# Kernel tuning notes

Measured on AMD Instinct MI355X. Metric: run time of the kernel, lower is better.

Reference implementation:

```python
import jax, jax.numpy as jnp
import numpy as np

HEAD_SIZE = 64
N_EMBD = 768

def setup_inputs() -> dict:
    key = jax.random.key(0)
    kx, kq, kk, kv = jax.random.split(key, 4)
    x = jax.random.normal(kx, (4, 4096, N_EMBD), dtype=jnp.float32)
    s = 1.0 / np.sqrt(N_EMBD)
    Wq = jax.random.normal(kq, (N_EMBD, HEAD_SIZE), dtype=jnp.float32) * s
    Wk = jax.random.normal(kk, (N_EMBD, HEAD_SIZE), dtype=jnp.float32) * s
    Wv = jax.random.normal(kv, (N_EMBD, HEAD_SIZE), dtype=jnp.float32) * s
    return {"x": x, "Wq": Wq, "Wk": Wk, "Wv": Wv}

def reference(x, Wq, Wk, Wv):
    b, t, c = x.shape
    h = Wq.shape[1]
    q = jnp.einsum('btc,ch->bth', x, Wq)
    k = jnp.einsum('btc,ch->bth', x, Wk)
    v = jnp.einsum('btc,ch->bth', x, Wv)
    scores = jnp.einsum('bqh,bkh->bqk', q, k) / jnp.sqrt(jnp.float32(h))
    causal = jnp.tril(jnp.ones((t, t), dtype=bool))  # [t,t]
    scores = jnp.where(causal, scores, -jnp.inf)
    attn = jax.nn.softmax(scores, axis=-1)
    return jnp.einsum('bqk,bkh->bqh', attn, v)
```

## Files before the change

### kernel.cpp

```cpp
#include <hip/hip_runtime.h>
#include <math.h>

#define BB 4
#define TT 4096
#define CC 768
#define HH 64
#define NN 192
#define LDP 72
#define GR 32
#define XSTR 776
#define SC2 0.180336880f

typedef __bf16 bf16x8 __attribute__((ext_vector_type(8)));
typedef float floatx4 __attribute__((ext_vector_type(4)));
typedef unsigned short u16x8 __attribute__((ext_vector_type(8)));

__device__ inline unsigned short f2bf(float f) {
    union { __bf16 b; unsigned short u; } v;
    v.b = (__bf16)f;
    return v.u;
}
__device__ inline float bf2f(unsigned short u) {
    union { unsigned int u; float f; } v;
    v.u = (unsigned int)u << 16;
    return v.f;
}

__global__ __launch_bounds__(256) void wprep(const float* __restrict__ Wq,
                                             const float* __restrict__ Wk,
                                             const float* __restrict__ Wv,
                                             unsigned short* __restrict__ wtf) {
    const int idx = blockIdx.x * 256 + threadIdx.x;
    if (idx >= NN * CC) return;
    const int j = idx & 7;
    const int lane = (idx >> 3) & 63;
    const int rest = idx >> 9;
    const int kg = rest % 24;
    const int n_tile = rest / 24;
    const int c = kg * 32 + (lane >> 4) * 8 + j;
    const int n = n_tile * 16 + (lane & 15);
    const float* W = (n < 64) ? Wq : (n < 128) ? Wk : Wv;
    wtf[idx] = f2bf(W[c * HH + (n & 63)]);
}

__global__ __launch_bounds__(256) void qkv_gemm(const float* __restrict__ x,
                                                const unsigned short* __restrict__ wtf,
                                                unsigned short* __restrict__ qb,
                                                unsigned short* __restrict__ kb,
                                                unsigned short* __restrict__ vbt) {
    __shared__ unsigned short As[GR * XSTR];

    const int tid = threadIdx.x;
    const int w = tid >> 6, lane = tid & 63;
    const int l15 = lane & 15, quad = lane >> 4;
    const int m0 = blockIdx.x * GR;
    const int n0 = w * 48;
    const int nt0 = w * 3;

    const float* xbase = x + (size_t)m0 * CC;
#pragma unroll
    for (int e = 0; e < 12; ++e) {
        const int c = tid + 256 * e;
        const int r = c / 96, off = (c - r * 96) * 8;
        const float4 v0 = *(const float4*)(xbase + (size_t)c * 8);
        const float4 v1 = *(const float4*)(xbase + (size_t)c * 8 + 4);
        u16x8 pk;
        pk[0] = f2bf(v0.x); pk[1] = f2bf(v0.y); pk[2] = f2bf(v0.z); pk[3] = f2bf(v0.w);
        pk[4] = f2bf(v1.x); pk[5] = f2bf(v1.y); pk[6] = f2bf(v1.z); pk[7] = f2bf(v1.w);
        *(u16x8*)(As + r * XSTR + off) = pk;
    }
    __syncthreads();

    floatx4 acc[2][3] = {};
#pragma unroll 4
    for (int step = 0; step < 12; ++step) {
        bf16x8 a0[2], a1[2];
#pragma unroll
        for (int rg = 0; rg < 2; ++rg) {
            const unsigned short* ap = As + (16 * rg + l15) * XSTR + step * 64 + quad * 8;
            a0[rg] = *(const bf16x8*)(ap);
            a1[rg] = *(const bf16x8*)(ap + 32);
        }
#pragma unroll
        for (int j = 0; j < 3; ++j) {
            const unsigned short* bp =
                wtf + ((size_t)((nt0 + j) * 24 + 2 * step) * 64 + lane) * 8;
            const bf16x8 b0 = *(const bf16x8*)(bp);
            const bf16x8 b1 = *(const bf16x8*)(bp + 512);
#pragma unroll
            for (int rg = 0; rg < 2; ++rg) {
                acc[rg][j] = __builtin_amdgcn_mfma_f32_16x16x32_bf16(a0[rg], b0, acc[rg][j], 0, 0, 0);
                acc[rg][j] = __builtin_amdgcn_mfma_f32_16x16x32_bf16(a1[rg], b1, acc[rg][j], 0, 0, 0);
            }
        }
    }

    const int b = m0 >> 12;
#pragma unroll
    for (int j = 0; j < 3; ++j) {
        const int n = n0 + j * 16 + l15;
        const int mid = n >> 6;
        const int h = n & 63;
#pragma unroll
        for (int rg = 0; rg < 2; ++rg) {
            const int tloc = (m0 & (TT - 1)) + 16 * rg + quad * 4;
            if (mid == 2) {
                ushort4 pk;
                pk.x = f2bf(acc[rg][j][0]); pk.y = f2bf(acc[rg][j][1]);
                pk.z = f2bf(acc[rg][j][2]); pk.w = f2bf(acc[rg][j][3]);
                *(ushort4*)(vbt + ((size_t)b * HH + h) * TT + tloc) = pk;
            } else {
                unsigned short* dst = (mid == 0) ? qb : kb;
#pragma unroll
                for (int r = 0; r < 4; ++r)
                    dst[(size_t)(m0 + 16 * rg + quad * 4 + r) * HH + h] = f2bf(acc[rg][j][r]);
            }
        }
    }
}

template<int CH>
__global__ __launch_bounds__(256) void attn_part(const unsigned short* __restrict__ qb,
                                                 const unsigned short* __restrict__ kb,
                                                 const unsigned short* __restrict__ vbt,
                                                 unsigned short* __restrict__ Opart,
                                                 float* __restrict__ lsum,
                                                 float* __restrict__ out) {
    __shared__ unsigned short Ks[64 * LDP];
    __shared__ unsigned short VTs[64 * LDP];
    __shared__ unsigned short Ps[4][16 * LDP];

    constexpr int NG = 64 / CH;
    constexpr int TOTB = CH * (NG * (NG + 1)) / 2;

    const int b = blockIdx.x & 3;
    int rem = TOTB - 1 - (blockIdx.x >> 2);
    int g = 0;
    while (rem >= CH * (g + 1)) { rem -= CH * (g + 1); ++g; }
    const int qt = g * CH + rem / (g + 1);
    const int ch = rem - (rem / (g + 1)) * (g + 1);

    const int q0  = qt * 64;
    const int tid = threadIdx.x;
    const int w = tid >> 6, lane = tid & 63;
    const int l15 = lane & 15, quad = lane >> 4;

    const unsigned short* Qb  = qb  + (size_t)b * TT * HH;
    const unsigned short* Kb  = kb  + (size_t)b * TT * HH;
    const unsigned short* VTb = vbt + (size_t)b * HH * TT;

    const int qrow = q0 + 16 * w + l15;
    const bf16x8 qf0 = *(const bf16x8*)(Qb + (size_t)qrow * HH + quad * 8);
    const bf16x8 qf1 = *(const bf16x8*)(Qb + (size_t)qrow * HH + 32 + quad * 8);

    floatx4 O[4] = {};
    floatx4 lacc = {0.f, 0.f, 0.f, 0.f};

    const int kt0 = ch * CH;
    const int kt1 = min(kt0 + CH, qt + 1);
    for (int kt = kt0; kt < kt1; ++kt) {
        __syncthreads();
        const unsigned short* Kt = Kb + (size_t)(kt * 64) * HH;
        const unsigned short* Vt = VTb + kt * 64;
#pragma unroll
        for (int e = 0; e < 2; ++e) {
            const int chunk = tid + 256 * e;
            const int r = chunk >> 3, c0 = (chunk & 7) * 8;
            *(u16x8*)(Ks + r * LDP + c0)  = *(const u16x8*)(Kt + r * HH + c0);
            *(u16x8*)(VTs + r * LDP + c0) = *(const u16x8*)(Vt + (size_t)r * TT + c0);
        }
        __syncthreads();

        floatx4 s[4];
#pragma unroll
        for (int ki = 0; ki < 4; ++ki) {
            const bf16x8 kf0 = *(const bf16x8*)(Ks + (16 * ki + l15) * LDP + quad * 8);
            const bf16x8 kf1 = *(const bf16x8*)(Ks + (16 * ki + l15) * LDP + 32 + quad * 8);
            floatx4 c = {};
            c = __builtin_amdgcn_mfma_f32_16x16x32_bf16(qf0, kf0, c, 0, 0, 0);
            c = __builtin_amdgcn_mfma_f32_16x16x32_bf16(qf1, kf1, c, 0, 0, 0);
            s[ki] = c * SC2;
        }

        if (kt == qt) {
#pragma unroll
            for (int ki = 0; ki < 4; ++ki)
#pragma unroll
                for (int r = 0; r < 4; ++r) {
                    const int kloc = 16 * ki + l15;
                    const int qloc = 16 * w + quad * 4 + r;
                    if (kloc > qloc) s[ki][r] = -INFINITY;
                }
        }

#pragma unroll
        for (int ki = 0; ki < 4; ++ki)
#pragma unroll
            for (int r = 0; r < 4; ++r) {
                const float p = exp2f(s[ki][r]);
                s[ki][r] = p;
                lacc[r] += p;
            }

        unsigned short* Pw = Ps[w];
#pragma unroll
        for (int ki = 0; ki < 4; ++ki)
#pragma unroll
            for (int r = 0; r < 4; ++r)
                Pw[(quad * 4 + r) * LDP + 16 * ki + l15] = f2bf(s[ki][r]);

        const bf16x8 pf0 = *(const bf16x8*)(Pw + l15 * LDP + quad * 8);
        const bf16x8 pf1 = *(const bf16x8*)(Pw + l15 * LDP + 32 + quad * 8);
#pragma unroll
        for (int di = 0; di < 4; ++di) {
            const bf16x8 vf0 = *(const bf16x8*)(VTs + (16 * di + l15) * LDP + quad * 8);
            const bf16x8 vf1 = *(const bf16x8*)(VTs + (16 * di + l15) * LDP + 32 + quad * 8);
            O[di] = __builtin_amdgcn_mfma_f32_16x16x32_bf16(pf0, vf0, O[di], 0, 0, 0);
            O[di] = __builtin_amdgcn_mfma_f32_16x16x32_bf16(pf1, vf1, O[di], 0, 0, 0);
        }
    }

    float l_r[4];
#pragma unroll
    for (int r = 0; r < 4; ++r) {
        float v = lacc[r];
#pragma unroll
        for (int msk = 8; msk >= 1; msk >>= 1) v += __shfl_xor(v, msk, 64);
        l_r[r] = v;
    }

    if (qt < CH) {
        float* outp = out + ((size_t)b * TT + q0 + 16 * w) * HH;
#pragma unroll
        for (int di = 0; di < 4; ++di)
#pragma unroll
            for (int r = 0; r < 4; ++r)
                outp[(quad * 4 + r) * HH + 16 * di + l15] = O[di][r] / l_r[r];
        return;
    }

    const int pbase = ((b * 64 + qt) * NG + ch) * 64;
    unsigned short* Op = Opart + (size_t)pbase * HH + 16 * w * HH;
#pragma unroll
    for (int di = 0; di < 4; ++di)
#pragma unroll
        for (int r = 0; r < 4; ++r)
            Op[(quad * 4 + r) * HH + 16 * di + l15] = f2bf(O[di][r]);
    if (l15 == 0) {
#pragma unroll
        for (int r = 0; r < 4; ++r)
            lsum[pbase + 16 * w + quad * 4 + r] = l_r[r];
    }
}

template<int CH>
__global__ __launch_bounds__(256) void attn_merge(const unsigned short* __restrict__ Opart,
                                                  const float* __restrict__ lsum,
                                                  float* __restrict__ out) {
    constexpr int NG = 64 / CH;
    const int g = blockIdx.x * 256 + threadIdx.x;
    const int row = g >> 3, oct = g & 7;
    const int b = row >> 12, t = row & (TT - 1);
    const int qt = t >> 6, rloc = t & 63;
    if (qt < CH) return;
    const int nchunk = qt / CH + 1;
    const int pbase = ((b * 64 + qt) * NG) * 64 + rloc;
    const int d0 = oct * 8;

    float L = 0.f;
    float a[8] = {};
    for (int c = 0; c < nchunk; ++c) {
        const int idx = pbase + c * 64;
        L += lsum[idx];
        const u16x8 pv = *(const u16x8*)(Opart + (size_t)idx * HH + d0);
#pragma unroll
        for (int k = 0; k < 8; ++k) a[k] += bf2f(pv[k]);
    }
    const float inv = 1.f / L;
    float4 o0, o1;
    o0.x = a[0] * inv; o0.y = a[1] * inv; o0.z = a[2] * inv; o0.w = a[3] * inv;
    o1.x = a[4] * inv; o1.y = a[5] * inv; o1.z = a[6] * inv; o1.w = a[7] * inv;
    float* dst = out + (size_t)row * HH + d0;
    *(float4*)(dst) = o0;
    *(float4*)(dst + 4) = o1;
}

__global__ __launch_bounds__(256) void attn_full(const unsigned short* __restrict__ qb,
                                                 const unsigned short* __restrict__ kb,
                                                 const unsigned short* __restrict__ vbt,
                                                 float* __restrict__ out) {
    __shared__ unsigned short Ks[64 * LDP];
    __shared__ unsigned short VTs[64 * LDP];
    __shared__ unsigned short Ps[4][16 * LDP];

    const int b   = blockIdx.x >> 6;
    const int qt  = blockIdx.x & 63;
    const int q0  = qt * 64;
    const int tid = threadIdx.x;
    const int w = tid >> 6, lane = tid & 63;
    const int l15 = lane & 15, quad = lane >> 4;

    const unsigned short* Qb  = qb  + (size_t)b * TT * HH;
    const unsigned short* Kb  = kb  + (size_t)b * TT * HH;
    const unsigned short* VTb = vbt + (size_t)b * HH * TT;

    const int qrow = q0 + 16 * w + l15;
    const bf16x8 qf0 = *(const bf16x8*)(Qb + (size_t)qrow * HH + quad * 8);
    const bf16x8 qf1 = *(const bf16x8*)(Qb + (size_t)qrow * HH + 32 + quad * 8);

    floatx4 O[4] = {};
    floatx4 lacc = {0.f, 0.f, 0.f, 0.f};

    for (int kt = 0; kt <= qt; ++kt) {
        __syncthreads();
        const unsigned short* Kt = Kb + (size_t)(kt * 64) * HH;
        const unsigned short* Vt = VTb + kt * 64;
#pragma unroll
        for (int e = 0; e < 2; ++e) {
            const int chunk = tid + 256 * e;
            const int r = chunk >> 3, c0 = (chunk & 7) * 8;
            *(u16x8*)(Ks + r * LDP + c0)  = *(const u16x8*)(Kt + r * HH + c0);
            *(u16x8*)(VTs + r * LDP + c0) = *(const u16x8*)(Vt + (size_t)r * TT + c0);
        }
        __syncthreads();

        floatx4 s[4];
#pragma unroll
        for (int ki = 0; ki < 4; ++ki) {
            const bf16x8 kf0 = *(const bf16x8*)(Ks + (16 * ki + l15) * LDP + quad * 8);
            const bf16x8 kf1 = *(const bf16x8*)(Ks + (16 * ki + l15) * LDP + 32 + quad * 8);
            floatx4 c = {};
            c = __builtin_amdgcn_mfma_f32_16x16x32_bf16(qf0, kf0, c, 0, 0, 0);
            c = __builtin_amdgcn_mfma_f32_16x16x32_bf16(qf1, kf1, c, 0, 0, 0);
            s[ki] = c * SC2;
        }
        if (kt == qt) {
#pragma unroll
            for (int ki = 0; ki < 4; ++ki)
#pragma unroll
                for (int r = 0; r < 4; ++r)
                    if (16 * ki + l15 > 16 * w + quad * 4 + r) s[ki][r] = -INFINITY;
        }
#pragma unroll
        for (int ki = 0; ki < 4; ++ki)
#pragma unroll
            for (int r = 0; r < 4; ++r) {
                const float p = exp2f(s[ki][r]);
                s[ki][r] = p; lacc[r] += p;
            }

        unsigned short* Pw = Ps[w];
#pragma unroll
        for (int ki = 0; ki < 4; ++ki)
#pragma unroll
            for (int r = 0; r < 4; ++r)
                Pw[(quad * 4 + r) * LDP + 16 * ki + l15] = f2bf(s[ki][r]);

        const bf16x8 pf0 = *(const bf16x8*)(Pw + l15 * LDP + quad * 8);
        const bf16x8 pf1 = *(const bf16x8*)(Pw + l15 * LDP + 32 + quad * 8);
#pragma unroll
        for (int di = 0; di < 4; ++di) {
            const bf16x8 vf0 = *(const bf16x8*)(VTs + (16 * di + l15) * LDP + quad * 8);
            const bf16x8 vf1 = *(const bf16x8*)(VTs + (16 * di + l15) * LDP + 32 + quad * 8);
            O[di] = __builtin_amdgcn_mfma_f32_16x16x32_bf16(pf0, vf0, O[di], 0, 0, 0);
            O[di] = __builtin_amdgcn_mfma_f32_16x16x32_bf16(pf1, vf1, O[di], 0, 0, 0);
        }
    }
    float l_r[4];
#pragma unroll
    for (int r = 0; r < 4; ++r) {
        float v = lacc[r];
#pragma unroll
        for (int msk = 8; msk >= 1; msk >>= 1) v += __shfl_xor(v, msk, 64);
        l_r[r] = v;
    }
    float* outp = out + ((size_t)b * TT + q0 + 16 * w) * HH;
#pragma unroll
    for (int di = 0; di < 4; ++di)
#pragma unroll
        for (int r = 0; r < 4; ++r)
            outp[(quad * 4 + r) * HH + 16 * di + l15] = O[di][r] / l_r[r];
}

extern "C" void kernel_launch(void* const* d_in, const int* in_sizes, int n_in,
                              void* d_out, int out_size, void* d_ws, size_t ws_size,
                              hipStream_t stream) {
    const float* x  = (const float*)d_in[0];
    const float* Wq = (const float*)d_in[1];
    const float* Wk = (const float*)d_in[2];
    const float* Wv = (const float*)d_in[3];
    float* out = (float*)d_out;

    const size_t nQKV = (size_t)BB * TT * HH;
    unsigned short* qb  = (unsigned short*)d_ws;
    unsigned short* kb  = qb + nQKV;
    unsigned short* vbt = kb + nQKV;
    unsigned short* wtf = vbt + nQKV;
    unsigned short* Opart = wtf + (size_t)NN * CC;

    const size_t prows8  = (size_t)BB * 64 * 8 * 64;
    const size_t prows16 = (size_t)BB * 64 * 4 * 64;
    float* lsum8  = (float*)(Opart + prows8 * HH);
    float* lsum16 = (float*)(Opart + prows16 * HH);
    const size_t need8  = (size_t)((char*)(lsum8  + prows8)  - (char*)d_ws);
    const size_t need16 = (size_t)((char*)(lsum16 + prows16) - (char*)d_ws);

    wprep<<<(NN * CC + 255) / 256, 256, 0, stream>>>(Wq, Wk, Wv, wtf);
    qkv_gemm<<<(BB * TT) / GR, 256, 0, stream>>>(x, wtf, qb, kb, vbt);
    if (ws_size >= need8) {
        attn_part<8><<<BB * 288, 256, 0, stream>>>(qb, kb, vbt, Opart, lsum8, out);
        attn_merge<8><<<(BB * TT * 8) / 256, 256, 0, stream>>>(Opart, lsum8, out);
    } else if (ws_size >= need16) {
        attn_part<16><<<BB * 160, 256, 0, stream>>>(qb, kb, vbt, Opart, lsum16, out);
        attn_merge<16><<<(BB * TT * 8) / 256, 256, 0, stream>>>(Opart, lsum16, out);
    } else {
        attn_full<<<BB * (TT / 64), 256, 0, stream>>>(qb, kb, vbt, out);
    }
}
```

Measured before the change: 130.6 us.

## Load K and V MFMA fragments directly from global memory, dropping LDS staging

Removes the shared-memory staging of K and V tiles and both block-wide barriers per key tile in the attention kernels. Each wave now reads its MFMA operand fragments straight from global memory (through L1/L2). This cuts the LDS round trip and the synchronization, and lowers LDS use, which may allow more resident blocks. In exchange, all four waves load the same K/V data redundantly from global memory, and the V reads stride by TT, so cache pressure and load latency go up with no explicit prefetching.

```diff
diff --git a/kernel.cpp b/kernel.cpp
--- a/kernel.cpp
+++ b/kernel.cpp
@@ -126,8 +126,6 @@
                                                  unsigned short* __restrict__ Opart,
                                                  float* __restrict__ lsum,
                                                  float* __restrict__ out) {
-    __shared__ unsigned short Ks[64 * LDP];
-    __shared__ unsigned short VTs[64 * LDP];
     __shared__ unsigned short Ps[4][16 * LDP];
 
     constexpr int NG = 64 / CH;
@@ -159,23 +157,15 @@
     const int kt0 = ch * CH;
     const int kt1 = min(kt0 + CH, qt + 1);
     for (int kt = kt0; kt < kt1; ++kt) {
-        __syncthreads();
         const unsigned short* Kt = Kb + (size_t)(kt * 64) * HH;
         const unsigned short* Vt = VTb + kt * 64;
-#pragma unroll
-        for (int e = 0; e < 2; ++e) {
-            const int chunk = tid + 256 * e;
-            const int r = chunk >> 3, c0 = (chunk & 7) * 8;
-            *(u16x8*)(Ks + r * LDP + c0)  = *(const u16x8*)(Kt + r * HH + c0);
-            *(u16x8*)(VTs + r * LDP + c0) = *(const u16x8*)(Vt + (size_t)r * TT + c0);
-        }
-        __syncthreads();
 
         floatx4 s[4];
 #pragma unroll
         for (int ki = 0; ki < 4; ++ki) {
-            const bf16x8 kf0 = *(const bf16x8*)(Ks + (16 * ki + l15) * LDP + quad * 8);
-            const bf16x8 kf1 = *(const bf16x8*)(Ks + (16 * ki + l15) * LDP + 32 + quad * 8);
+            const unsigned short* kp = Kt + (size_t)(16 * ki + l15) * HH + quad * 8;
+            const bf16x8 kf0 = *(const bf16x8*)(kp);
+            const bf16x8 kf1 = *(const bf16x8*)(kp + 32);
             floatx4 c = {};
             c = __builtin_amdgcn_mfma_f32_16x16x32_bf16(qf0, kf0, c, 0, 0, 0);
             c = __builtin_amdgcn_mfma_f32_16x16x32_bf16(qf1, kf1, c, 0, 0, 0);
@@ -213,8 +203,9 @@
         const bf16x8 pf1 = *(const bf16x8*)(Pw + l15 * LDP + 32 + quad * 8);
 #pragma unroll
         for (int di = 0; di < 4; ++di) {
-            const bf16x8 vf0 = *(const bf16x8*)(VTs + (16 * di + l15) * LDP + quad * 8);
-            const bf16x8 vf1 = *(const bf16x8*)(VTs + (16 * di + l15) * LDP + 32 + quad * 8);
+            const unsigned short* vp = Vt + (size_t)(16 * di + l15) * TT + quad * 8;
+            const bf16x8 vf0 = *(const bf16x8*)(vp);
+            const bf16x8 vf1 = *(const bf16x8*)(vp + 32);
             O[di] = __builtin_amdgcn_mfma_f32_16x16x32_bf16(pf0, vf0, O[di], 0, 0, 0);
             O[di] = __builtin_amdgcn_mfma_f32_16x16x32_bf16(pf1, vf1, O[di], 0, 0, 0);
         }
@@ -289,8 +280,6 @@
                                                  const unsigned short* __restrict__ kb,
                                                  const unsigned short* __restrict__ vbt,
                                                  float* __restrict__ out) {
-    __shared__ unsigned short Ks[64 * LDP];
-    __shared__ unsigned short VTs[64 * LDP];
     __shared__ unsigned short Ps[4][16 * LDP];
 
     const int b   = blockIdx.x >> 6;
@@ -312,23 +301,15 @@
     floatx4 lacc = {0.f, 0.f, 0.f, 0.f};
 
     for (int kt = 0; kt <= qt; ++kt) {
-        __syncthreads();
         const unsigned short* Kt = Kb + (size_t)(kt * 64) * HH;
         const unsigned short* Vt = VTb + kt * 64;
-#pragma unroll
-        for (int e = 0; e < 2; ++e) {
-            const int chunk = tid + 256 * e;
-            const int r = chunk >> 3, c0 = (chunk & 7) * 8;
-            *(u16x8*)(Ks + r * LDP + c0)  = *(const u16x8*)(Kt + r * HH + c0);
-            *(u16x8*)(VTs + r * LDP + c0) = *(const u16x8*)(Vt + (size_t)r * TT + c0);
-        }
-        __syncthreads();
 
         floatx4 s[4];
 #pragma unroll
         for (int ki = 0; ki < 4; ++ki) {
-            const bf16x8 kf0 = *(const bf16x8*)(Ks + (16 * ki + l15) * LDP + quad * 8);
-            const bf16x8 kf1 = *(const bf16x8*)(Ks + (16 * ki + l15) * LDP + 32 + quad * 8);
+            const unsigned short* kp = Kt + (size_t)(16 * ki + l15) * HH + quad * 8;
+            const bf16x8 kf0 = *(const bf16x8*)(kp);
+            const bf16x8 kf1 = *(const bf16x8*)(kp + 32);
             floatx4 c = {};
             c = __builtin_amdgcn_mfma_f32_16x16x32_bf16(qf0, kf0, c, 0, 0, 0);
             c = __builtin_amdgcn_mfma_f32_16x16x32_bf16(qf1, kf1, c, 0, 0, 0);
@@ -360,8 +341,9 @@
         const bf16x8 pf1 = *(const bf16x8*)(Pw + l15 * LDP + 32 + quad * 8);
 #pragma unroll
         for (int di = 0; di < 4; ++di) {
-            const bf16x8 vf0 = *(const bf16x8*)(VTs + (16 * di + l15) * LDP + quad * 8);
-            const bf16x8 vf1 = *(const bf16x8*)(VTs + (16 * di + l15) * LDP + 32 + quad * 8);
+            const unsigned short* vp = Vt + (size_t)(16 * di + l15) * TT + quad * 8;
+            const bf16x8 vf0 = *(const bf16x8*)(vp);
+            const bf16x8 vf1 = *(const bf16x8*)(vp + 32);
             O[di] = __builtin_amdgcn_mfma_f32_16x16x32_bf16(pf0, vf0, O[di], 0, 0, 0);
             O[di] = __builtin_amdgcn_mfma_f32_16x16x32_bf16(pf1, vf1, O[di], 0, 0, 0);
         }
```

Result: slower. 175.6 us (+34.5%).

## Rework attention partial kernel to 32x32 MFMA with register-resident K/V and split-K waves

Applied to the files above, without the earlier changes.

Replaces the 16x16x32 MFMA attention tile with 32x32x16 MFMAs computing S^T = K·Q^T. K and V fragments now load straight from global memory into registers, with the next K tile prefetched, so the shared-memory staging and the two barriers per tile are gone. P is repacked in registers using packed bf16 converts and a cross-half lane shuffle instead of a shared-memory round trip. The 4 waves are split 2x2 over query and key halves, and their partial O and row sums are reduced through shared memory at the end. This removes LDS traffic and synchronisation, at the cost of redundant global reads of K/V per wave and more register pressure.

```diff
diff --git a/kernel.cpp b/kernel.cpp
--- a/kernel.cpp
+++ b/kernel.cpp
@@ -13,6 +13,7 @@
 
 typedef __bf16 bf16x8 __attribute__((ext_vector_type(8)));
 typedef float floatx4 __attribute__((ext_vector_type(4)));
+typedef float floatx16 __attribute__((ext_vector_type(16)));
 typedef unsigned short u16x8 __attribute__((ext_vector_type(8)));
 
 __device__ inline unsigned short f2bf(float f) {
@@ -24,6 +25,11 @@
     union { unsigned int u; float f; } v;
     v.u = (unsigned int)u << 16;
     return v.f;
+}
+__device__ inline unsigned cvtpk(float lo, float hi) {
+    unsigned d;
+    asm("v_cvt_pk_bf16_f32 %0, %1, %2" : "=v"(d) : "v"(lo), "v"(hi));
+    return d;
 }
 
 __global__ __launch_bounds__(256) void wprep(const float* __restrict__ Wq,
@@ -126,9 +132,8 @@
                                                  unsigned short* __restrict__ Opart,
                                                  float* __restrict__ lsum,
                                                  float* __restrict__ out) {
-    __shared__ unsigned short Ks[64 * LDP];
-    __shared__ unsigned short VTs[64 * LDP];
-    __shared__ unsigned short Ps[4][16 * LDP];
+    __shared__ float Osh[2][2][16][64];
+    __shared__ float Lsh[2][64];
 
     constexpr int NG = 64 / CH;
     constexpr int TOTB = CH * (NG * (NG + 1)) / 2;
@@ -143,114 +148,140 @@
     const int q0  = qt * 64;
     const int tid = threadIdx.x;
     const int w = tid >> 6, lane = tid & 63;
-    const int l15 = lane & 15, quad = lane >> 4;
+    const int wq = w >> 1, wk = w & 1;
+    const int l31 = lane & 31, hi = lane >> 5;
 
     const unsigned short* Qb  = qb  + (size_t)b * TT * HH;
     const unsigned short* Kb  = kb  + (size_t)b * TT * HH;
     const unsigned short* VTb = vbt + (size_t)b * HH * TT;
 
-    const int qrow = q0 + 16 * w + l15;
-    const bf16x8 qf0 = *(const bf16x8*)(Qb + (size_t)qrow * HH + quad * 8);
-    const bf16x8 qf1 = *(const bf16x8*)(Qb + (size_t)qrow * HH + 32 + quad * 8);
-
-    floatx4 O[4] = {};
-    floatx4 lacc = {0.f, 0.f, 0.f, 0.f};
+    bf16x8 qf[4];
+    {
+        const unsigned short* qp = Qb + (size_t)(q0 + 32 * wq + l31) * HH + 8 * hi;
+#pragma unroll
+        for (int s = 0; s < 4; ++s) qf[s] = *(const bf16x8*)(qp + 16 * s);
+    }
+
+    floatx16 o0 = {}, o1 = {};
+    float lacc = 0.f;
 
     const int kt0 = ch * CH;
     const int kt1 = min(kt0 + CH, qt + 1);
+
+    const unsigned short* kbase = Kb + (size_t)(32 * wk + l31) * HH + 8 * hi;
+    bf16x8 kn[4];
+#pragma unroll
+    for (int s = 0; s < 4; ++s)
+        kn[s] = *(const bf16x8*)(kbase + (size_t)kt0 * 64 * HH + 16 * s);
+
     for (int kt = kt0; kt < kt1; ++kt) {
-        __syncthreads();
-        const unsigned short* Kt = Kb + (size_t)(kt * 64) * HH;
-        const unsigned short* Vt = VTb + kt * 64;
-#pragma unroll
-        for (int e = 0; e < 2; ++e) {
-            const int chunk = tid + 256 * e;
-            const int r = chunk >> 3, c0 = (chunk & 7) * 8;
-            *(u16x8*)(Ks + r * LDP + c0)  = *(const u16x8*)(Kt + r * HH + c0);
-            *(u16x8*)(VTs + r * LDP + c0) = *(const u16x8*)(Vt + (size_t)r * TT + c0);
-        }
-        __syncthreads();
-
-        floatx4 s[4];
-#pragma unroll
-        for (int ki = 0; ki < 4; ++ki) {
-            const bf16x8 kf0 = *(const bf16x8*)(Ks + (16 * ki + l15) * LDP + quad * 8);
-            const bf16x8 kf1 = *(const bf16x8*)(Ks + (16 * ki + l15) * LDP + 32 + quad * 8);
-            floatx4 c = {};
-            c = __builtin_amdgcn_mfma_f32_16x16x32_bf16(qf0, kf0, c, 0, 0, 0);
-            c = __builtin_amdgcn_mfma_f32_16x16x32_bf16(qf1, kf1, c, 0, 0, 0);
-            s[ki] = c * SC2;
-        }
+        bf16x8 kc[4];
+#pragma unroll
+        for (int s = 0; s < 4; ++s) kc[s] = kn[s];
+
+        bf16x8 vv[4];
+#pragma unroll
+        for (int i = 0; i < 4; ++i) {
+            const int db = i >> 1, m = i & 1;
+            vv[i] = *(const bf16x8*)(VTb + (size_t)(32 * db + l31) * TT
+                                     + kt * 64 + 32 * wk + 16 * m + 8 * hi);
+        }
+        if (kt + 1 < kt1) {
+#pragma unroll
+            for (int s = 0; s < 4; ++s)
+                kn[s] = *(const bf16x8*)(kbase + (size_t)(kt + 1) * 64 * HH + 16 * s);
+        }
+
+        floatx16 sa = {};
+#pragma unroll
+        for (int s = 0; s < 4; ++s)
+            sa = __builtin_amdgcn_mfma_f32_32x32x16_bf16(kc[s], qf[s], sa, 0, 0, 0);
+
+        float st[16];
+#pragma unroll
+        for (int r = 0; r < 16; ++r) st[r] = sa[r] * SC2;
 
         if (kt == qt) {
-#pragma unroll
-            for (int ki = 0; ki < 4; ++ki)
-#pragma unroll
-                for (int r = 0; r < 4; ++r) {
-                    const int kloc = 16 * ki + l15;
-                    const int qloc = 16 * w + quad * 4 + r;
-                    if (kloc > qloc) s[ki][r] = -INFINITY;
-                }
-        }
-
-#pragma unroll
-        for (int ki = 0; ki < 4; ++ki)
-#pragma unroll
-            for (int r = 0; r < 4; ++r) {
-                const float p = exp2f(s[ki][r]);
-                s[ki][r] = p;
-                lacc[r] += p;
+            const int qloc = 32 * wq + l31;
+#pragma unroll
+            for (int r = 0; r < 16; ++r) {
+                const int kloc = 32 * wk + (r & 3) + 8 * (r >> 2) + 4 * hi;
+                if (kloc > qloc) st[r] = -INFINITY;
             }
-
-        unsigned short* Pw = Ps[w];
-#pragma unroll
-        for (int ki = 0; ki < 4; ++ki)
-#pragma unroll
-            for (int r = 0; r < 4; ++r)
-                Pw[(quad * 4 + r) * LDP + 16 * ki + l15] = f2bf(s[ki][r]);
-
-        const bf16x8 pf0 = *(const bf16x8*)(Pw + l15 * LDP + quad * 8);
-        const bf16x8 pf1 = *(const bf16x8*)(Pw + l15 * LDP + 32 + quad * 8);
-#pragma unroll
-        for (int di = 0; di < 4; ++di) {
-            const bf16x8 vf0 = *(const bf16x8*)(VTs + (16 * di + l15) * LDP + quad * 8);
-            const bf16x8 vf1 = *(const bf16x8*)(VTs + (16 * di + l15) * LDP + 32 + quad * 8);
-            O[di] = __builtin_amdgcn_mfma_f32_16x16x32_bf16(pf0, vf0, O[di], 0, 0, 0);
-            O[di] = __builtin_amdgcn_mfma_f32_16x16x32_bf16(pf1, vf1, O[di], 0, 0, 0);
-        }
-    }
-
-    float l_r[4];
-#pragma unroll
-    for (int r = 0; r < 4; ++r) {
-        float v = lacc[r];
-#pragma unroll
-        for (int msk = 8; msk >= 1; msk >>= 1) v += __shfl_xor(v, msk, 64);
-        l_r[r] = v;
-    }
+        }
+
+#pragma unroll
+        for (int r = 0; r < 16; ++r) {
+            const float p = exp2f(st[r]);
+            st[r] = p;
+            lacc += p;
+        }
+
+        bf16x8 pf[2];
+#pragma unroll
+        for (int m = 0; m < 2; ++m) {
+            const unsigned d0 = cvtpk(st[8 * m + 0], st[8 * m + 1]);
+            const unsigned d1 = cvtpk(st[8 * m + 2], st[8 * m + 3]);
+            const unsigned d2 = cvtpk(st[8 * m + 4], st[8 * m + 5]);
+            const unsigned d3 = cvtpk(st[8 * m + 6], st[8 * m + 7]);
+            const unsigned e0 = (unsigned)__shfl_xor((int)d0, 32);
+            const unsigned e1 = (unsigned)__shfl_xor((int)d1, 32);
+            const unsigned e2 = (unsigned)__shfl_xor((int)d2, 32);
+            const unsigned e3 = (unsigned)__shfl_xor((int)d3, 32);
+            union { unsigned u[4]; bf16x8 v; } pk;
+            pk.u[0] = hi ? e2 : d0;
+            pk.u[1] = hi ? e3 : d1;
+            pk.u[2] = hi ? d2 : e0;
+            pk.u[3] = hi ? d3 : e1;
+            pf[m] = pk.v;
+        }
+
+        o0 = __builtin_amdgcn_mfma_f32_32x32x16_bf16(vv[0], pf[0], o0, 0, 0, 0);
+        o0 = __builtin_amdgcn_mfma_f32_32x32x16_bf16(vv[1], pf[1], o0, 0, 0, 0);
+        o1 = __builtin_amdgcn_mfma_f32_32x32x16_bf16(vv[2], pf[0], o1, 0, 0, 0);
+        o1 = __builtin_amdgcn_mfma_f32_32x32x16_bf16(vv[3], pf[1], o1, 0, 0, 0);
+    }
+
+    if (wk == 1) {
+#pragma unroll
+        for (int r = 0; r < 16; ++r) {
+            Osh[wq][0][r][lane] = o0[r];
+            Osh[wq][1][r][lane] = o1[r];
+        }
+        Lsh[wq][lane] = lacc;
+    }
+    __syncthreads();
+    if (wk == 1) return;
+#pragma unroll
+    for (int r = 0; r < 16; ++r) {
+        o0[r] += Osh[wq][0][r][lane];
+        o1[r] += Osh[wq][1][r][lane];
+    }
+    lacc += Lsh[wq][lane];
+    const float l = lacc + __shfl_xor(lacc, 32);
 
     if (qt < CH) {
-        float* outp = out + ((size_t)b * TT + q0 + 16 * w) * HH;
-#pragma unroll
-        for (int di = 0; di < 4; ++di)
-#pragma unroll
-            for (int r = 0; r < 4; ++r)
-                outp[(quad * 4 + r) * HH + 16 * di + l15] = O[di][r] / l_r[r];
+        float* outp = out + ((size_t)b * TT + q0 + 32 * wq + l31) * HH;
+        const float inv = 1.f / l;
+#pragma unroll
+        for (int r = 0; r < 16; ++r) {
+            const int dd = (r & 3) + 8 * (r >> 2) + 4 * hi;
+            outp[dd]      = o0[r] * inv;
+            outp[32 + dd] = o1[r] * inv;
+        }
         return;
     }
 
     const int pbase = ((b * 64 + qt) * NG + ch) * 64;
-    unsigned short* Op = Opart + (size_t)pbase * HH + 16 * w * HH;
-#pragma unroll
-    for (int di = 0; di < 4; ++di)
-#pragma unroll
-        for (int r = 0; r < 4; ++r)
-            Op[(quad * 4 + r) * HH + 16 * di + l15] = f2bf(O[di][r]);
-    if (l15 == 0) {
-#pragma unroll
-        for (int r = 0; r < 4; ++r)
-            lsum[pbase + 16 * w + quad * 4 + r] = l_r[r];
-    }
+    unsigned short* Op = Opart + ((size_t)pbase + 32 * wq + l31) * HH;
+#pragma unroll
+    for (int a = 0; a < 4; ++a) {
+        *(unsigned*)(Op + 8 * a + 4 * hi)          = cvtpk(o0[4 * a + 0], o0[4 * a + 1]);
+        *(unsigned*)(Op + 8 * a + 4 * hi + 2)      = cvtpk(o0[4 * a + 2], o0[4 * a + 3]);
+        *(unsigned*)(Op + 32 + 8 * a + 4 * hi)     = cvtpk(o1[4 * a + 0], o1[4 * a + 1]);
+        *(unsigned*)(Op + 32 + 8 * a + 4 * hi + 2) = cvtpk(o1[4 * a + 2], o1[4 * a + 3]);
+    }
+    if (hi == 0) lsum[pbase + 32 * wq + l31] = l;
 }
 
 template<int CH>
```

New measurement: 144.9 us. 11.0% more time.
